# Kernel optimization log

Hardware: AMD Instinct MI355X
Metric: run time of the kernel (lower is better)

Reference implementation:

```python
import jax, jax.numpy as jnp
import numpy as np

EMB, HEADS, T_BLK = 1024, 16, 2048
B, T = 2, 2048
HD = EMB // HEADS


def setup_inputs() -> dict:
    key = jax.random.key(0)
    ks = jax.random.split(key, 9)
    s = 1.0 / np.sqrt(EMB)
    return {
        "x": jax.random.normal(ks[0], (B, T, EMB), jnp.float32),
        "Wq": jax.random.normal(ks[1], (EMB, EMB), jnp.float32) * s,
        "bq": jax.random.normal(ks[2], (EMB,), jnp.float32) * s,
        "Wk": jax.random.normal(ks[3], (EMB, EMB), jnp.float32) * s,
        "bk": jax.random.normal(ks[4], (EMB,), jnp.float32) * s,
        "Wv": jax.random.normal(ks[5], (EMB, EMB), jnp.float32) * s,
        "bv": jax.random.normal(ks[6], (EMB,), jnp.float32) * s,
        "Wo": jax.random.normal(ks[7], (EMB, EMB), jnp.float32) * s,
        "bo": jax.random.normal(ks[8], (EMB,), jnp.float32) * s,
    }


def reference(x, Wq, bq, Wk, bk, Wv, bv, Wo, bo):
    # eval mode: dropout is identity
    Bn, Tn, C = x.shape
    def proj(W, b):
        y = x @ W.T + b                      # [B,T,C]
        return y.reshape(Bn, Tn, HEADS, HD).transpose(0, 2, 1, 3)  # [B,H,T,hd]
    q, k, v = proj(Wq, bq), proj(Wk, bk), proj(Wv, bv)
    scores = jnp.einsum('bhqd,bhkd->bhqk', q, k) * (HD ** -0.5)  # [B,H,T,T]
    causal = jnp.tril(jnp.ones((Tn, Tn), dtype=bool))
    scores = jnp.where(causal, scores, -jnp.inf)
    w = jax.nn.softmax(scores, axis=-1)
    out = jnp.einsum('bhqk,bhkd->bhqd', w, v)                    # [B,H,T,hd]
    out = out.transpose(0, 2, 1, 3).reshape(Bn, Tn, C)
    return out @ Wo.T + bo
```

## Files before the change

kernel.cpp:

```cpp
#include <hip/hip_runtime.h>
#include <stdint.h>

#define EMB   1024
#define HEADS 16
#define HD    64
#define BB    2
#define TT    2048
#define MTOT  (BB*TT)
#define LDA   72
#define LDP   72

#define ELX (4194304u)
#define ELW (1048576u)

#define CSCALE (0.125f * 1.44269504088896f)

typedef __attribute__((ext_vector_type(8))) short short8;
typedef __attribute__((ext_vector_type(4))) float f32x4;
typedef __attribute__((ext_vector_type(4))) unsigned short us4;

__device__ __forceinline__ float bf2f(ushort u) {
  union { uint32_t u; float f; } x; x.u = ((uint32_t)u) << 16; return x.f;
}
__device__ __forceinline__ ushort f2bf(float f) {
  union { float f; uint32_t u; } x; x.f = f;
  uint32_t u = x.u;
  u += 0x7fffu + ((u >> 16) & 1u);
  return (ushort)(u >> 16);
}
__device__ __forceinline__ uint32_t pack2(uint32_t lo, uint32_t hi) {
  return (lo >> 16) | (hi & 0xFFFF0000u);
}
__device__ __forceinline__ short8 pack8(f32x4 a, f32x4 b) {
  union { f32x4 v; uint32_t u[4]; } A, B;
  A.v = a; B.v = b;
  union { uint32_t d[4]; short8 s; } R;
  R.d[0] = pack2(A.u[0], A.u[1]);
  R.d[1] = pack2(A.u[2], A.u[3]);
  R.d[2] = pack2(B.u[0], B.u[1]);
  R.d[3] = pack2(B.u[2], B.u[3]);
  return R.s;
}
__device__ __forceinline__ short8 cvt8_rne(const float* f) {
  f32x4 a = *(const f32x4*)f;
  f32x4 b = *(const f32x4*)(f + 4);
  short8 r;
  r[0] = (short)f2bf(a[0]); r[1] = (short)f2bf(a[1]);
  r[2] = (short)f2bf(a[2]); r[3] = (short)f2bf(a[3]);
  r[4] = (short)f2bf(b[0]); r[5] = (short)f2bf(b[1]);
  r[6] = (short)f2bf(b[2]); r[7] = (short)f2bf(b[3]);
  return r;
}

__global__ void detect_dtype(const uint32_t* __restrict__ x, int* __restrict__ flag) {
  const int lane = threadIdx.x & 63;
  int cnt = 0;
#pragma unroll
  for (int i = 0; i < 4; ++i) {
    const uint32_t v = x[lane * 4 + i];
    const uint32_t e = ((v & 0xFFFFu) >> 7) & 0xFFu;
    cnt += (e >= 0x70u && e <= 0x8Fu) ? 1 : 0;
  }
#pragma unroll
  for (int off = 1; off < 64; off <<= 1) cnt += __shfl_xor(cnt, off);
  if (lane == 0) *flag = (cnt > 128) ? 1 : 0;
}

__global__ __launch_bounds__(256) void convert3(const void* __restrict__ w0,
                                                const void* __restrict__ w1,
                                                const void* __restrict__ w2,
                                                ushort* __restrict__ dst,
                                                const int* __restrict__ flag) {
  const size_t i = ((size_t)blockIdx.x * 256 + threadIdx.x) * 8;
  const int wi = (int)(i >> 20);
  const size_t off = i & (ELW - 1);
  const void* src = (wi == 0) ? w0 : (wi == 1) ? w1 : w2;
  if (*flag) *(short8*)(dst + i) = *(const short8*)((const ushort*)src + off);
  else       *(short8*)(dst + i) = cvt8_rne((const float*)src + off);
}

template<bool ABF>
__device__ __forceinline__ void gemm_qkv64(const void* __restrict__ Ap,
                                           const ushort* __restrict__ Wp,
                                           int m0, int n0,
                                           ushort* As, ushort* Ws,
                                           f32x4 acc[4][2]) {
  const int tid  = threadIdx.x;
  const int w    = tid >> 6;
  const int lane = tid & 63;
  const int quad = lane >> 4;
  const int l16  = lane & 15;
  const int arow = tid >> 2;
  const int acol = (tid & 3) * 16;
  const int brow = tid >> 1;
  const int bcol = (tid & 1) * 32;

  const size_t aoff = (size_t)(m0 + arow) * EMB + acol;
  const size_t boff = (size_t)(n0 + brow) * EMB + bcol;

  short8 ab[3][2];
  f32x4  af[3][4];
  short8 wb[3][4];

#pragma unroll
  for (int s = 0; s < 2; ++s) {
    if constexpr (ABF) {
      ab[s][0] = *(const short8*)((const ushort*)Ap + aoff + 64 * s);
      ab[s][1] = *(const short8*)((const ushort*)Ap + aoff + 64 * s + 8);
    } else {
#pragma unroll
      for (int i = 0; i < 4; ++i)
        af[s][i] = *(const f32x4*)((const float*)Ap + aoff + 64 * s + 4 * i);
    }
#pragma unroll
    for (int i = 0; i < 4; ++i)
      wb[s][i] = *(const short8*)(Wp + boff + 64 * s + 8 * i);
  }

#pragma unroll
  for (int it = 0; it < 16; ++it) {
    const int k0 = it * 64;
    const int cur = it % 3, nxt = (it + 2) % 3;
    __syncthreads();
    if constexpr (ABF) {
      *(short8*)&As[arow * LDP + acol]     = ab[cur][0];
      *(short8*)&As[arow * LDP + acol + 8] = ab[cur][1];
    } else {
      *(short8*)&As[arow * LDP + acol]     = pack8(af[cur][0], af[cur][1]);
      *(short8*)&As[arow * LDP + acol + 8] = pack8(af[cur][2], af[cur][3]);
    }
#pragma unroll
    for (int i = 0; i < 4; ++i) *(short8*)&Ws[brow * LDP + bcol + 8 * i] = wb[cur][i];
    if (it + 2 < 16) {
      const int kn = k0 + 128;
      if constexpr (ABF) {
        ab[nxt][0] = *(const short8*)((const ushort*)Ap + aoff + kn);
        ab[nxt][1] = *(const short8*)((const ushort*)Ap + aoff + kn + 8);
      } else {
#pragma unroll
        for (int i = 0; i < 4; ++i)
          af[nxt][i] = *(const f32x4*)((const float*)Ap + aoff + kn + 4 * i);
      }
#pragma unroll
      for (int i = 0; i < 4; ++i)
        wb[nxt][i] = *(const short8*)(Wp + boff + kn + 8 * i);
    }
    __syncthreads();

#pragma unroll
    for (int ks = 0; ks < 2; ++ks) {
      short8 a_[4], b_[2];
#pragma unroll
      for (int i = 0; i < 4; ++i)
        a_[i] = *(const short8*)&As[(i * 16 + l16) * LDP + ks * 32 + quad * 8];
#pragma unroll
      for (int i = 0; i < 2; ++i)
        b_[i] = *(const short8*)&Ws[(w * 32 + i * 16 + l16) * LDP + ks * 32 + quad * 8];
#pragma unroll
      for (int mi = 0; mi < 4; ++mi)
#pragma unroll
        for (int ni = 0; ni < 2; ++ni)
          acc[mi][ni] = __builtin_amdgcn_mfma_f32_16x16x32_bf16(a_[mi], b_[ni], acc[mi][ni], 0, 0, 0);
    }
  }
}

__device__ __forceinline__ void qkv_epi64(f32x4 acc[4][2], int mt, int n0, int mat,
                                          const void* bias, int isbf,
                                          ushort* qo, ushort* ko, ushort* vo) {
  const int tid  = threadIdx.x;
  const int w    = tid >> 6;
  const int lane = tid & 63;
  const int quad = lane >> 4;
  const int l16  = lane & 15;
  ushort* dst = (mat == 0) ? qo : ko;
  const float sc = (mat == 0) ? CSCALE : 1.0f;

#pragma unroll
  for (int ni = 0; ni < 2; ++ni) {
    const int n = n0 + w * 32 + ni * 16 + l16;
    const float bv_ = isbf ? bf2f(((const ushort*)bias)[n]) : ((const float*)bias)[n];
    const int hh = n >> 6, d = n & 63;
#pragma unroll
    for (int mi = 0; mi < 4; ++mi) {
      const int mbase = mt * 64 + mi * 16 + quad * 4;
      const int b = mbase >> 11, t = mbase & (TT - 1);
      if (mat == 2) {
        us4 pk;
#pragma unroll
        for (int r = 0; r < 4; ++r) pk[r] = f2bf(acc[mi][ni][r] + bv_);
        *(us4*)&vo[((size_t)((b * HEADS + hh) * HD + d)) * TT + t] = pk;
      } else {
#pragma unroll
        for (int r = 0; r < 4; ++r)
          dst[((size_t)((b * HEADS + hh) * TT + t + r)) * HD + d] = f2bf((acc[mi][ni][r] + bv_) * sc);
      }
    }
  }
}

__global__ __launch_bounds__(256) void qkv_pipe(const void* __restrict__ x,
                                                const ushort* __restrict__ w3,
                                                const void* __restrict__ bq,
                                                const void* __restrict__ bk,
                                                const void* __restrict__ bv,
                                                ushort* __restrict__ qo,
                                                ushort* __restrict__ ko,
                                                ushort* __restrict__ vo,
                                                const int* __restrict__ flag) {
  __shared__ __align__(16) ushort As[64 * LDP];
  __shared__ __align__(16) ushort Ws[128 * LDP];
  const int xcd = blockIdx.x & 7;
  const int i   = blockIdx.x >> 3;
  const int nt  = xcd * 3 + (i % 3);
  const int mt  = i / 3;
  const int mat = nt >> 3;
  const int n0  = (nt & 7) * 128;
  const ushort* W  = w3 + (size_t)mat * ELW;
  const void* bias = (mat == 0) ? bq : (mat == 1) ? bk : bv;

  f32x4 acc[4][2];
#pragma unroll
  for (int a = 0; a < 4; ++a)
#pragma unroll
    for (int b = 0; b < 2; ++b) acc[a][b] = (f32x4){0.f, 0.f, 0.f, 0.f};

  const int isbf = *flag;
  if (isbf) gemm_qkv64<true >(x, W, mt * 64, n0, As, Ws, acc);
  else      gemm_qkv64<false>(x, W, mt * 64, n0, As, Ws, acc);
  qkv_epi64(acc, mt, n0, mat, bias, isbf, qo, ko, vo);
}

__global__ __launch_bounds__(256) void attn3(const ushort* __restrict__ qw,
                                             const ushort* __restrict__ kw,
                                             const ushort* __restrict__ vtw,
                                             ushort* __restrict__ out) {
  __shared__ __align__(16) ushort Ks[64 * LDA];
  __shared__ __align__(16) ushort Vts[64 * LDA];
  __shared__ __align__(16) ushort Ps[4][16 * LDA];

  const int bid = blockIdx.x;
  const int j  = bid >> 8;
  const int r8 = bid & 255;
  const int qh = r8 & 31;
  const int bh = j * 8 + (r8 >> 5);
  int qt;
  if      (j == 0) qt = qh;
  else if (j == 1) qt = 31 - qh;
  else if (j == 2) qt = (qh + 16) & 31;
  else             qt = 31 - ((qh + 16) & 31);
  const int h = bh & (HEADS - 1);
  const int b = bh >> 4;

  const int tid  = threadIdx.x;
  const int w    = tid >> 6;
  const int lane = tid & 63;
  const int quad = lane >> 4;
  const int l16  = lane & 15;

  const size_t hoff = ((size_t)(b * HEADS + h)) * TT * HD;
  const ushort* Qg = qw + hoff;
  const ushort* Kg = kw + hoff;
  const ushort* Vg = vtw + hoff;
  const int q0 = qt * 64;

  short8 qf[2];
  {
    const ushort* qrow = Qg + (size_t)(q0 + w * 16 + l16) * HD;
    qf[0] = *(const short8*)(qrow + quad * 8);
    qf[1] = *(const short8*)(qrow + 32 + quad * 8);
  }

  const int row = tid >> 2;
  const int c0  = (tid & 3) * 16;
  const ushort* Kbase = Kg + (size_t)row * HD + c0;
  const ushort* Vbase = Vg + (size_t)row * TT + c0;

  float lsp[4] = {0.f, 0.f, 0.f, 0.f};
  f32x4 O[4];
#pragma unroll
  for (int ni = 0; ni < 4; ++ni) O[ni] = (f32x4){0.f, 0.f, 0.f, 0.f};

  auto compute_tile = [&](int kt) {
    f32x4 s[4];
#pragma unroll
    for (int ni = 0; ni < 4; ++ni) s[ni] = (f32x4){0.f, 0.f, 0.f, 0.f};
#pragma unroll
    for (int ks = 0; ks < 2; ++ks) {
#pragma unroll
      for (int ni = 0; ni < 4; ++ni) {
        short8 kb = *(const short8*)&Ks[(ni * 16 + l16) * LDA + ks * 32 + quad * 8];
        s[ni] = __builtin_amdgcn_mfma_f32_16x16x32_bf16(kb, qf[ks], s[ni], 0, 0, 0);
      }
    }
    if (kt == qt) {
      const int qq = w * 16 + l16;
#pragma unroll
      for (int ni = 0; ni < 4; ++ni) {
#pragma unroll
        for (int r = 0; r < 4; ++r)
          if (ni * 16 + quad * 4 + r > qq) s[ni][r] = -__builtin_inff();
      }
    }
#pragma unroll
    for (int ni = 0; ni < 4; ++ni) {
      union { float f; uint32_t u; } p0, p1, p2, p3;
      p0.f = exp2f(s[ni][0]); p1.f = exp2f(s[ni][1]);
      p2.f = exp2f(s[ni][2]); p3.f = exp2f(s[ni][3]);
      lsp[ni] += (p0.f + p1.f) + (p2.f + p3.f);
      uint2 dw;
      dw.x = pack2(p0.u, p1.u);
      dw.y = pack2(p2.u, p3.u);
      *(uint2*)&Ps[w][l16 * LDA + ni * 16 + quad * 4] = dw;
    }
#pragma unroll
    for (int ks = 0; ks < 2; ++ks) {
      short8 a = *(const short8*)&Ps[w][l16 * LDA + ks * 32 + quad * 8];
#pragma unroll
      for (int ni = 0; ni < 4; ++ni) {
        short8 vb = *(const short8*)&Vts[(ni * 16 + l16) * LDA + ks * 32 + quad * 8];
        O[ni] = __builtin_amdgcn_mfma_f32_16x16x32_bf16(a, vb, O[ni], 0, 0, 0);
      }
    }
  };

  short8 ak0, ak1, av0, av1;
  short8 bk0, bk1, bv0, bv1;
  ak0 = *(const short8*)(Kbase);
  ak1 = *(const short8*)(Kbase + 8);
  av0 = *(const short8*)(Vbase);
  av1 = *(const short8*)(Vbase + 8);

  for (int kt = 0; kt <= qt; ) {
    __syncthreads();
    *(short8*)&Ks[row * LDA + c0]      = ak0;
    *(short8*)&Ks[row * LDA + c0 + 8]  = ak1;
    *(short8*)&Vts[row * LDA + c0]     = av0;
    *(short8*)&Vts[row * LDA + c0 + 8] = av1;
    if (kt + 1 <= qt) {
      const size_t ko_ = (size_t)(kt + 1) * 64 * HD;
      bk0 = *(const short8*)(Kbase + ko_);
      bk1 = *(const short8*)(Kbase + ko_ + 8);
      bv0 = *(const short8*)(Vbase + (kt + 1) * 64);
      bv1 = *(const short8*)(Vbase + (kt + 1) * 64 + 8);
    }
    __syncthreads();
    compute_tile(kt);
    ++kt;
    if (kt > qt) break;

    __syncthreads();
    *(short8*)&Ks[row * LDA + c0]      = bk0;
    *(short8*)&Ks[row * LDA + c0 + 8]  = bk1;
    *(short8*)&Vts[row * LDA + c0]     = bv0;
    *(short8*)&Vts[row * LDA + c0 + 8] = bv1;
    if (kt + 1 <= qt) {
      const size_t ko_ = (size_t)(kt + 1) * 64 * HD;
      ak0 = *(const short8*)(Kbase + ko_);
      ak1 = *(const short8*)(Kbase + ko_ + 8);
      av0 = *(const short8*)(Vbase + (kt + 1) * 64);
      av1 = *(const short8*)(Vbase + (kt + 1) * 64 + 8);
    }
    __syncthreads();
    compute_tile(kt);
    ++kt;
  }

  float lst = (lsp[0] + lsp[1]) + (lsp[2] + lsp[3]);
  lst += __shfl_xor(lst, 16);
  lst += __shfl_xor(lst, 32);

#pragma unroll
  for (int r = 0; r < 4; ++r) {
    const float inv = 1.0f / __shfl(lst, (lane & 48) | (quad * 4 + r));
    const int t = q0 + w * 16 + quad * 4 + r;
#pragma unroll
    for (int ni = 0; ni < 4; ++ni) {
      out[((size_t)(b * TT + t)) * EMB + h * HD + ni * 16 + l16] = f2bf(O[ni][r] * inv);
    }
  }
}

template<bool WBF>
__device__ __forceinline__ void proj_core(const ushort* __restrict__ A,
                                          const void* __restrict__ Wo,
                                          int m0, int n0,
                                          ushort* As, ushort* Ws,
                                          f32x4 acc[2][4]) {
  const int tid  = threadIdx.x;
  const int w    = tid >> 6;
  const int lane = tid & 63;
  const int quad = lane >> 4;
  const int l16  = lane & 15;
  const int arow = tid >> 1;
  const int acol = (tid & 1) * 32;
  const int brow = tid >> 2;
  const int bcol = (tid & 3) * 16;

  const size_t aoff = (size_t)(m0 + arow) * EMB + acol;
  const size_t boff = (size_t)(n0 + brow) * EMB + bcol;

  short8 ab[3][4];
  short8 wb[3][2];
  f32x4  wf[3][4];

#pragma unroll
  for (int s = 0; s < 2; ++s) {
#pragma unroll
    for (int i = 0; i < 4; ++i)
      ab[s][i] = *(const short8*)(A + aoff + 64 * s + 8 * i);
    if constexpr (WBF) {
      wb[s][0] = *(const short8*)((const ushort*)Wo + boff + 64 * s);
      wb[s][1] = *(const short8*)((const ushort*)Wo + boff + 64 * s + 8);
    } else {
#pragma unroll
      for (int i = 0; i < 4; ++i)
        wf[s][i] = *(const f32x4*)((const float*)Wo + boff + 64 * s + 4 * i);
    }
  }

#pragma unroll
  for (int it = 0; it < 16; ++it) {
    const int k0 = it * 64;
    const int cur = it % 3, nxt = (it + 2) % 3;
    __syncthreads();
#pragma unroll
    for (int i = 0; i < 4; ++i)
      *(short8*)&As[arow * LDP + acol + 8 * i] = ab[cur][i];
    if constexpr (WBF) {
      *(short8*)&Ws[brow * LDP + bcol]     = wb[cur][0];
      *(short8*)&Ws[brow * LDP + bcol + 8] = wb[cur][1];
    } else {
      *(short8*)&Ws[brow * LDP + bcol]     = pack8(wf[cur][0], wf[cur][1]);
      *(short8*)&Ws[brow * LDP + bcol + 8] = pack8(wf[cur][2], wf[cur][3]);
    }
    if (it + 2 < 16) {
      const int kn = k0 + 128;
#pragma unroll
      for (int i = 0; i < 4; ++i)
        ab[nxt][i] = *(const short8*)(A + aoff + kn + 8 * i);
      if constexpr (WBF) {
        wb[nxt][0] = *(const short8*)((const ushort*)Wo + boff + kn);
        wb[nxt][1] = *(const short8*)((const ushort*)Wo + boff + kn + 8);
      } else {
#pragma unroll
        for (int i = 0; i < 4; ++i)
          wf[nxt][i] = *(const f32x4*)((const float*)Wo + boff + kn + 4 * i);
      }
    }
    __syncthreads();

#pragma unroll
    for (int ks = 0; ks < 2; ++ks) {
      short8 a_[2], b_[4];
#pragma unroll
      for (int i = 0; i < 2; ++i)
        a_[i] = *(const short8*)&As[(w * 32 + i * 16 + l16) * LDP + ks * 32 + quad * 8];
#pragma unroll
      for (int i = 0; i < 4; ++i)
        b_[i] = *(const short8*)&Ws[(i * 16 + l16) * LDP + ks * 32 + quad * 8];
#pragma unroll
      for (int mi = 0; mi < 2; ++mi)
#pragma unroll
        for (int ni = 0; ni < 4; ++ni)
          acc[mi][ni] = __builtin_amdgcn_mfma_f32_16x16x32_bf16(a_[mi], b_[ni], acc[mi][ni], 0, 0, 0);
    }
  }
}

__global__ __launch_bounds__(256) void proj_pipe(const ushort* __restrict__ A,
                                                 const void* __restrict__ Wo,
                                                 const void* __restrict__ bo,
                                                 void* __restrict__ out,
                                                 const int* __restrict__ flag) {
  __shared__ __align__(16) ushort As[128 * LDP];
  __shared__ __align__(16) ushort Ws[64 * LDP];
  const int nt = blockIdx.x & 15;
  const int mt = blockIdx.x >> 4;
  const int n0 = nt * 64;
  const int m0 = mt * 128;

  f32x4 acc[2][4];
#pragma unroll
  for (int i = 0; i < 2; ++i)
#pragma unroll
    for (int jj = 0; jj < 4; ++jj) acc[i][jj] = (f32x4){0.f, 0.f, 0.f, 0.f};

  const int isbf = *flag;
  if (isbf) proj_core<true >(A, Wo, m0, n0, As, Ws, acc);
  else      proj_core<false>(A, Wo, m0, n0, As, Ws, acc);

  const int tid  = threadIdx.x;
  const int w    = tid >> 6;
  const int lane = tid & 63;
  const int quad = lane >> 4;
  const int l16  = lane & 15;

#pragma unroll
  for (int ni = 0; ni < 4; ++ni) {
    const int n = n0 + ni * 16 + l16;
    const float bv_ = isbf ? bf2f(((const ushort*)bo)[n]) : ((const float*)bo)[n];
#pragma unroll
    for (int mi = 0; mi < 2; ++mi) {
#pragma unroll
      for (int r = 0; r < 4; ++r) {
        const int m = m0 + w * 32 + mi * 16 + quad * 4 + r;
        const float v = acc[mi][ni][r] + bv_;
        if (isbf) ((ushort*)out)[(size_t)m * EMB + n] = f2bf(v);
        else      ((float*) out)[(size_t)m * EMB + n] = v;
      }
    }
  }
}

extern "C" void kernel_launch(void* const* d_in, const int* in_sizes, int n_in,
                              void* d_out, int out_size, void* d_ws, size_t ws_size,
                              hipStream_t stream) {
  const void* x  = d_in[0];
  const void* Wq = d_in[1];
  const void* bq = d_in[2];
  const void* Wk = d_in[3];
  const void* bk = d_in[4];
  const void* Wv = d_in[5];
  const void* bv = d_in[6];
  const void* Wo = d_in[7];
  const void* bo = d_in[8];

  int* flag = (int*)d_ws;
  ushort* base = (ushort*)((char*)d_ws + 256);

  ushort* q_ws  = base;
  ushort* k_ws  = q_ws + ELX;
  ushort* vt_ws = k_ws + ELX;
  ushort* w3    = vt_ws + ELX;
  ushort* o_ws  = vt_ws + ELX;

  detect_dtype<<<dim3(1), dim3(64), 0, stream>>>((const uint32_t*)x, flag);
  convert3<<<dim3(1536), dim3(256), 0, stream>>>(Wq, Wk, Wv, w3, flag);
  qkv_pipe<<<dim3(1536), dim3(256), 0, stream>>>(x, w3, bq, bk, bv,
                                                 q_ws, k_ws, vt_ws, flag);
  attn3<<<dim3(1024), dim3(256), 0, stream>>>(q_ws, k_ws, vt_ws, o_ws);
  proj_pipe<<<dim3(512), dim3(256), 0, stream>>>(o_ws, Wo, bo, d_out, flag);
}
```

Measured before the change: 218.2 us.

## Enlarge QKV GEMM tiles to 128x128 with direct global-to-LDS loads and XOR swizzle

The QKV projection GEMM moves from 64x128 tiles to 128x128 tiles, with each wave computing a 64x64 sub-tile, halving the grid. Weight tiles (and x when bf16) are loaded with global_load_lds straight into an XOR-swizzled unpadded LDS layout instead of going through registers. For fp32 x, only a one-stage register prefetch is kept. This raises arithmetic intensity and cuts register staging, but drops the previous 3-stage register pipeline, so load latency is less hidden and occupancy may fall from higher accumulator register use.

```diff
diff --git a/kernel.cpp b/kernel.cpp
--- a/kernel.cpp
+++ b/kernel.cpp
@@ -50,6 +50,12 @@
   r[4] = (short)f2bf(b[0]); r[5] = (short)f2bf(b[1]);
   r[6] = (short)f2bf(b[2]); r[7] = (short)f2bf(b[3]);
   return r;
+}
+
+__device__ __forceinline__ void gll16(const void* g, void* l) {
+  __builtin_amdgcn_global_load_lds((const __attribute__((address_space(1))) void*)g,
+                                   (__attribute__((address_space(3))) void*)l,
+                                   16, 0, 0);
 }
 
 __global__ void detect_dtype(const uint32_t* __restrict__ x, int* __restrict__ flag) {
@@ -80,121 +86,78 @@
 }
 
 template<bool ABF>
-__device__ __forceinline__ void gemm_qkv64(const void* __restrict__ Ap,
-                                           const ushort* __restrict__ Wp,
-                                           int m0, int n0,
-                                           ushort* As, ushort* Ws,
-                                           f32x4 acc[4][2]) {
+__device__ __forceinline__ void qkv_core(const void* __restrict__ xp,
+                                         const ushort* __restrict__ W,
+                                         int m0, int n0r,
+                                         ushort* As, ushort* Bs,
+                                         f32x4 acc[4][4]) {
   const int tid  = threadIdx.x;
   const int w    = tid >> 6;
   const int lane = tid & 63;
   const int quad = lane >> 4;
   const int l16  = lane & 15;
-  const int arow = tid >> 2;
-  const int acol = (tid & 3) * 16;
-  const int brow = tid >> 1;
-  const int bcol = (tid & 1) * 32;
-
-  const size_t aoff = (size_t)(m0 + arow) * EMB + acol;
-  const size_t boff = (size_t)(n0 + brow) * EMB + bcol;
-
-  short8 ab[3][2];
-  f32x4  af[3][4];
-  short8 wb[3][4];
-
-#pragma unroll
-  for (int s = 0; s < 2; ++s) {
-    if constexpr (ABF) {
-      ab[s][0] = *(const short8*)((const ushort*)Ap + aoff + 64 * s);
-      ab[s][1] = *(const short8*)((const ushort*)Ap + aoff + 64 * s + 8);
-    } else {
-#pragma unroll
-      for (int i = 0; i < 4; ++i)
-        af[s][i] = *(const f32x4*)((const float*)Ap + aoff + 64 * s + 4 * i);
-    }
-#pragma unroll
-    for (int i = 0; i < 4; ++i)
-      wb[s][i] = *(const short8*)(Wp + boff + 64 * s + 8 * i);
-  }
-
-#pragma unroll
+  const int wr   = w >> 1, wc = w & 1;
+
+  const int srow = tid >> 3;
+  const int scol = (tid & 7) ^ (srow & 7);
+  const size_t aoff = (size_t)(m0 + srow) * EMB + scol * 8;
+  const size_t boff = (size_t)(n0r + srow) * EMB + scol * 8;
+
+  f32x4 ar[8];
+  if constexpr (!ABF) {
+    const float* xf = (const float*)xp;
+#pragma unroll
+    for (int j = 0; j < 4; ++j) {
+      ar[2 * j]     = *(const f32x4*)(xf + aoff + (size_t)j * 32 * EMB);
+      ar[2 * j + 1] = *(const f32x4*)(xf + aoff + (size_t)j * 32 * EMB + 4);
+    }
+  }
+
+  const int rsw = l16 & 7;
+
   for (int it = 0; it < 16; ++it) {
     const int k0 = it * 64;
-    const int cur = it % 3, nxt = (it + 2) % 3;
     __syncthreads();
     if constexpr (ABF) {
-      *(short8*)&As[arow * LDP + acol]     = ab[cur][0];
-      *(short8*)&As[arow * LDP + acol + 8] = ab[cur][1];
+      const ushort* xu = (const ushort*)xp;
+#pragma unroll
+      for (int j = 0; j < 4; ++j)
+        gll16(xu + aoff + (size_t)j * 32 * EMB + k0, As + j * 2048 + w * 512);
     } else {
-      *(short8*)&As[arow * LDP + acol]     = pack8(af[cur][0], af[cur][1]);
-      *(short8*)&As[arow * LDP + acol + 8] = pack8(af[cur][2], af[cur][3]);
-    }
-#pragma unroll
-    for (int i = 0; i < 4; ++i) *(short8*)&Ws[brow * LDP + bcol + 8 * i] = wb[cur][i];
-    if (it + 2 < 16) {
-      const int kn = k0 + 128;
-      if constexpr (ABF) {
-        ab[nxt][0] = *(const short8*)((const ushort*)Ap + aoff + kn);
-        ab[nxt][1] = *(const short8*)((const ushort*)Ap + aoff + kn + 8);
-      } else {
-#pragma unroll
-        for (int i = 0; i < 4; ++i)
-          af[nxt][i] = *(const f32x4*)((const float*)Ap + aoff + kn + 4 * i);
-      }
-#pragma unroll
-      for (int i = 0; i < 4; ++i)
-        wb[nxt][i] = *(const short8*)(Wp + boff + kn + 8 * i);
+#pragma unroll
+      for (int j = 0; j < 4; ++j)
+        *(short8*)&As[((size_t)j * 256 + tid) * 8] = pack8(ar[2 * j], ar[2 * j + 1]);
+    }
+#pragma unroll
+    for (int j = 0; j < 4; ++j)
+      gll16(W + boff + (size_t)j * 32 * EMB + k0, Bs + j * 2048 + w * 512);
+    if constexpr (!ABF) {
+      if (it + 1 < 16) {
+        const float* xf = (const float*)xp;
+#pragma unroll
+        for (int j = 0; j < 4; ++j) {
+          ar[2 * j]     = *(const f32x4*)(xf + aoff + (size_t)j * 32 * EMB + k0 + 64);
+          ar[2 * j + 1] = *(const f32x4*)(xf + aoff + (size_t)j * 32 * EMB + k0 + 68);
+        }
+      }
     }
     __syncthreads();
 
 #pragma unroll
     for (int ks = 0; ks < 2; ++ks) {
-      short8 a_[4], b_[2];
-#pragma unroll
-      for (int i = 0; i < 4; ++i)
-        a_[i] = *(const short8*)&As[(i * 16 + l16) * LDP + ks * 32 + quad * 8];
-#pragma unroll
-      for (int i = 0; i < 2; ++i)
-        b_[i] = *(const short8*)&Ws[(w * 32 + i * 16 + l16) * LDP + ks * 32 + quad * 8];
+      const int pc = (ks * 4 + quad) ^ rsw;
+      short8 a_[4], b_[4];
 #pragma unroll
       for (int mi = 0; mi < 4; ++mi)
-#pragma unroll
-        for (int ni = 0; ni < 2; ++ni)
+        a_[mi] = *(const short8*)&As[(wr * 64 + mi * 16 + l16) * 64 + pc * 8];
+#pragma unroll
+      for (int ni = 0; ni < 4; ++ni)
+        b_[ni] = *(const short8*)&Bs[(wc * 64 + ni * 16 + l16) * 64 + pc * 8];
+#pragma unroll
+      for (int mi = 0; mi < 4; ++mi)
+#pragma unroll
+        for (int ni = 0; ni < 4; ++ni)
           acc[mi][ni] = __builtin_amdgcn_mfma_f32_16x16x32_bf16(a_[mi], b_[ni], acc[mi][ni], 0, 0, 0);
-    }
-  }
-}
-
-__device__ __forceinline__ void qkv_epi64(f32x4 acc[4][2], int mt, int n0, int mat,
-                                          const void* bias, int isbf,
-                                          ushort* qo, ushort* ko, ushort* vo) {
-  const int tid  = threadIdx.x;
-  const int w    = tid >> 6;
-  const int lane = tid & 63;
-  const int quad = lane >> 4;
-  const int l16  = lane & 15;
-  ushort* dst = (mat == 0) ? qo : ko;
-  const float sc = (mat == 0) ? CSCALE : 1.0f;
-
-#pragma unroll
-  for (int ni = 0; ni < 2; ++ni) {
-    const int n = n0 + w * 32 + ni * 16 + l16;
-    const float bv_ = isbf ? bf2f(((const ushort*)bias)[n]) : ((const float*)bias)[n];
-    const int hh = n >> 6, d = n & 63;
-#pragma unroll
-    for (int mi = 0; mi < 4; ++mi) {
-      const int mbase = mt * 64 + mi * 16 + quad * 4;
-      const int b = mbase >> 11, t = mbase & (TT - 1);
-      if (mat == 2) {
-        us4 pk;
-#pragma unroll
-        for (int r = 0; r < 4; ++r) pk[r] = f2bf(acc[mi][ni][r] + bv_);
-        *(us4*)&vo[((size_t)((b * HEADS + hh) * HD + d)) * TT + t] = pk;
-      } else {
-#pragma unroll
-        for (int r = 0; r < 4; ++r)
-          dst[((size_t)((b * HEADS + hh) * TT + t + r)) * HD + d] = f2bf((acc[mi][ni][r] + bv_) * sc);
-      }
     }
   }
 }
@@ -208,27 +171,59 @@
                                                 ushort* __restrict__ ko,
                                                 ushort* __restrict__ vo,
                                                 const int* __restrict__ flag) {
-  __shared__ __align__(16) ushort As[64 * LDP];
-  __shared__ __align__(16) ushort Ws[128 * LDP];
-  const int xcd = blockIdx.x & 7;
-  const int i   = blockIdx.x >> 3;
+  __shared__ __align__(16) ushort As[128 * 64];
+  __shared__ __align__(16) ushort Bs[128 * 64];
+  const int bid = blockIdx.x;
+  const int xcd = bid & 7;
+  const int i   = bid >> 3;
   const int nt  = xcd * 3 + (i % 3);
   const int mt  = i / 3;
   const int mat = nt >> 3;
-  const int n0  = (nt & 7) * 128;
+  const int n0r = (nt & 7) * 128;
+  const int m0  = mt * 128;
   const ushort* W  = w3 + (size_t)mat * ELW;
   const void* bias = (mat == 0) ? bq : (mat == 1) ? bk : bv;
 
-  f32x4 acc[4][2];
+  f32x4 acc[4][4];
 #pragma unroll
   for (int a = 0; a < 4; ++a)
 #pragma unroll
-    for (int b = 0; b < 2; ++b) acc[a][b] = (f32x4){0.f, 0.f, 0.f, 0.f};
+    for (int b = 0; b < 4; ++b) acc[a][b] = (f32x4){0.f, 0.f, 0.f, 0.f};
 
   const int isbf = *flag;
-  if (isbf) gemm_qkv64<true >(x, W, mt * 64, n0, As, Ws, acc);
-  else      gemm_qkv64<false>(x, W, mt * 64, n0, As, Ws, acc);
-  qkv_epi64(acc, mt, n0, mat, bias, isbf, qo, ko, vo);
+  if (isbf) qkv_core<true >(x, W, m0, n0r, As, Bs, acc);
+  else      qkv_core<false>(x, W, m0, n0r, As, Bs, acc);
+
+  const int tid  = threadIdx.x;
+  const int w    = tid >> 6;
+  const int lane = tid & 63;
+  const int quad = lane >> 4;
+  const int l16  = lane & 15;
+  const int wr   = w >> 1, wc = w & 1;
+  ushort* dst = (mat == 0) ? qo : ko;
+  const float sc = (mat == 0) ? CSCALE : 1.0f;
+
+#pragma unroll
+  for (int ni = 0; ni < 4; ++ni) {
+    const int n = n0r + wc * 64 + ni * 16 + l16;
+    const float bv_ = isbf ? bf2f(((const ushort*)bias)[n]) : ((const float*)bias)[n];
+    const int h = n >> 6, d = n & 63;
+#pragma unroll
+    for (int mi = 0; mi < 4; ++mi) {
+      const int mbase = m0 + wr * 64 + mi * 16 + quad * 4;
+      const int b = mbase >> 11, t = mbase & (TT - 1);
+      if (mat == 2) {
+        us4 pk;
+#pragma unroll
+        for (int r = 0; r < 4; ++r) pk[r] = f2bf(acc[mi][ni][r] + bv_);
+        *(us4*)&vo[((size_t)((b * HEADS + h) * HD + d)) * TT + t] = pk;
+      } else {
+#pragma unroll
+        for (int r = 0; r < 4; ++r)
+          dst[((size_t)((b * HEADS + h) * TT + t + r)) * HD + d] = f2bf((acc[mi][ni][r] + bv_) * sc);
+      }
+    }
+  }
 }
 
 __global__ __launch_bounds__(256) void attn3(const ushort* __restrict__ qw,
@@ -537,8 +532,8 @@
 
   detect_dtype<<<dim3(1), dim3(64), 0, stream>>>((const uint32_t*)x, flag);
   convert3<<<dim3(1536), dim3(256), 0, stream>>>(Wq, Wk, Wv, w3, flag);
-  qkv_pipe<<<dim3(1536), dim3(256), 0, stream>>>(x, w3, bq, bk, bv,
-                                                 q_ws, k_ws, vt_ws, flag);
+  qkv_pipe<<<dim3(768), dim3(256), 0, stream>>>(x, w3, bq, bk, bv,
+                                                q_ws, k_ws, vt_ws, flag);
   attn3<<<dim3(1024), dim3(256), 0, stream>>>(q_ws, k_ws, vt_ws, o_ws);
   proj_pipe<<<dim3(512), dim3(256), 0, stream>>>(o_ws, Wo, bo, d_out, flag);
 }
```

Result: no change. 217.3 us (-0.4%).
